# Kernel tuning notes

Measured on AMD Instinct MI355X. Metric: run time of the kernel, lower is better.

Reference implementation:

```python
import jax, jax.numpy as jnp
import numpy as np

B, CIN, COUT, H, W = 8, 64, 64, 32, 64


def _conv3x3(x, w, b):
    # x: [B,Cin,H,W], w: [Cout,Cin,3,3], b: [Cout]; SAME padding (pad=1)
    y = jax.lax.conv_general_dilated(
        x, w, window_strides=(1, 1), padding=((1, 1), (1, 1)),
        dimension_numbers=('NCHW', 'OIHW', 'NCHW'))
    return y + b[None, :, None, None]


def setup_inputs() -> dict:
    key = jax.random.key(0)
    ks = jax.random.split(key, 7)
    fan_in = CIN * 3 * 3
    s = 1.0 / np.sqrt(fan_in)
    x = jax.random.normal(ks[0], (B, CIN, H, W), dtype=jnp.float32)
    wq = jax.random.uniform(ks[1], (COUT, CIN, 3, 3), jnp.float32, -s, s)
    bq = jax.random.uniform(ks[2], (COUT,), jnp.float32, -s, s)
    wk = jax.random.uniform(ks[3], (COUT, CIN, 3, 3), jnp.float32, -s, s)
    bk = jax.random.uniform(ks[4], (COUT,), jnp.float32, -s, s)
    wv = jax.random.uniform(ks[5], (COUT, CIN, 3, 3), jnp.float32, -s, s)
    bv = jax.random.uniform(ks[6], (COUT,), jnp.float32, -s, s)
    return {"x": x, "wq": wq, "bq": bq, "wk": wk, "bk": bk, "wv": wv, "bv": bv}


def reference(x, wq, bq, wk, bk, wv, bv):
    b, _, h, w = x.shape
    n = h * w
    q = _conv3x3(x, wq, bq).reshape(b, COUT, n)  # [B,C,N]
    k = _conv3x3(x, wk, bk).reshape(b, COUT, n)
    v = _conv3x3(x, wv, bv).reshape(b, COUT, n)
    # scores[b, i, j] = sum_c q[b,c,i] * k[b,c,j]  (NOTE: no 1/sqrt(d) scaling, as in source)
    scores = jnp.einsum('bci,bcj->bij', q, k)      # [B,N,N]
    attn = jax.nn.softmax(scores, axis=-1)
    out = jnp.einsum('bij,bcj->bci', attn, v)      # attn @ V^T, then transpose -> [B,C,N]
    return out.reshape(b, COUT, h, w)
```

## Files before the change

### kernel.cpp

```cpp
#include <hip/hip_runtime.h>
#include <hip/hip_bf16.h>

#define BATCH 8
#define NC    64
#define HH    32
#define WW    64
#define NN    2048
#define NCP   72
#define NCHUNK 4
#define KVBLK 64

typedef __attribute__((ext_vector_type(8))) short bf16x8;
typedef __attribute__((ext_vector_type(4))) short short4v;
typedef __attribute__((ext_vector_type(4))) float f32x4;

__device__ __forceinline__ unsigned short f2bf(float f) {
    union { float f; unsigned u; } v; v.f = f;
    unsigned r = v.u + 0x7fffu + ((v.u >> 16) & 1u);
    return (unsigned short)(r >> 16);
}
__device__ __forceinline__ float bf2f(unsigned short h) {
    union { unsigned u; float f; } v; v.u = ((unsigned)h) << 16;
    return v.f;
}

__device__ __forceinline__ bf16x8 load8(const unsigned short* a, const unsigned short* b) {
    short4v lo = *(const short4v*)a;
    short4v hi = *(const short4v*)b;
    return __builtin_shufflevector(lo, hi, 0, 1, 2, 3, 4, 5, 6, 7);
}

__device__ __forceinline__ int ci_of_slot(int j) {
    return (j & 32) | (((j >> 2) & 1) << 4) | (((j >> 3) & 3) << 2) | (j & 3);
}

__global__ __launch_bounds__(256) void prep_w(
    const float* __restrict__ wq, const float* __restrict__ wk,
    const float* __restrict__ wv, unsigned short* __restrict__ wb)
{
    const int idx = blockIdx.x * 256 + threadIdx.x;
    if (idx >= 9 * 192 * 64) return;
    const int j    = idx & 63;
    const int row  = (idx >> 6) % 192;
    const int tap  = idx / (192 * 64);
    const int ci   = ci_of_slot(j);
    const int conv = row >> 6;
    const int cout = row & 63;
    const float* ww = (conv == 0) ? wq : (conv == 1) ? wk : wv;
    wb[idx] = f2bf(ww[((size_t)cout * 64 + ci) * 9 + tap]);
}

__global__ __launch_bounds__(256) void prep_x(
    const float* __restrict__ x, unsigned short* __restrict__ xb)
{
    __shared__ unsigned short T[64][72];
    const int bi  = blockIdx.x >> 5;
    const int y   = blockIdx.x & 31;
    const int tid = threadIdx.x;

#pragma unroll
    for (int pass = 0; pass < 16; ++pass) {
        const int idx = pass * 256 + tid;
        const int ci = idx >> 6, xx = idx & 63;
        T[xx][ci] = f2bf(x[(((size_t)bi * 64 + ci) * 32 + y) * 64 + xx]);
    }
    __syncthreads();

#pragma unroll
    for (int pass = 0; pass < 2; ++pass) {
        const int chunk = pass * 256 + tid;
        const int xx = chunk >> 3, j8 = chunk & 7;
        unsigned short h[8];
#pragma unroll
        for (int e = 0; e < 8; ++e)
            h[e] = T[xx][ci_of_slot(j8 * 8 + e)];
        uint4 u;
        u.x = (unsigned)h[0] | ((unsigned)h[1] << 16);
        u.y = (unsigned)h[2] | ((unsigned)h[3] << 16);
        u.z = (unsigned)h[4] | ((unsigned)h[5] << 16);
        u.w = (unsigned)h[6] | ((unsigned)h[7] << 16);
        *(uint4*)(xb + ((((size_t)bi * 32 + y) * 64 + xx) * 64) + j8 * 8) = u;
    }
}

__global__ __launch_bounds__(256) void conv_mfma(
    const unsigned short* __restrict__ xb,
    const unsigned short* __restrict__ wb,
    const float* __restrict__ bq, const float* __restrict__ bk,
    const float* __restrict__ bv,
    unsigned short* __restrict__ qT,
    unsigned short* __restrict__ kT,
    unsigned short* __restrict__ vv)
{
    __shared__ __align__(16) unsigned short Xs[3][66][NCP];
    __shared__ __align__(16) unsigned short Ws[2][96][NCP];

    const int bid = blockIdx.x;
    const int bi  = bid >> 6;
    const int rem = bid & 63;
    const int y   = rem >> 1;
    const int h   = rem & 1;
    const int tid = threadIdx.x;
    const int l   = tid & 63;
    const int w   = tid >> 6;
    const int g   = l >> 4;
    const int li  = l & 15;
    const int mq  = w & 1;
    const int pp  = w >> 1;

#pragma unroll
    for (int r = 0; r < 3; ++r) {
        const int yy = y + r - 1;
#pragma unroll
        for (int pass = 0; pass < 3; ++pass) {
            const int chunk = pass * 256 + tid;
            if (chunk >= 528) break;
            const int c = chunk >> 3, ci8 = chunk & 7;
            uint4 d = {0, 0, 0, 0};
            const int xx = c - 1;
            if (yy >= 0 && yy < HH && xx >= 0 && xx < WW)
                d = *(const uint4*)(xb + ((((size_t)bi * HH + yy) * WW + xx) * 64) + ci8 * 8);
            *(uint4*)&Xs[r][c][ci8 * 8] = d;
        }
    }
#pragma unroll
    for (int pass = 0; pass < 3; ++pass) {
        const int chunk = pass * 256 + tid;
        const int row = chunk >> 3, ci8 = chunk & 7;
        uint4 d = *(const uint4*)(wb + ((size_t)(h * 96 + row)) * 64 + ci8 * 8);
        *(uint4*)&Ws[0][row][ci8 * 8] = d;
    }
    __syncthreads();

    f32x4 acc[2][3];
#pragma unroll
    for (int p2 = 0; p2 < 2; ++p2)
#pragma unroll
        for (int ct = 0; ct < 3; ++ct) acc[p2][ct] = (f32x4){0, 0, 0, 0};

#pragma unroll
    for (int tap = 0; tap < 9; ++tap) {
        const int ky = tap / 3, kx = tap % 3;
        const int cur = tap & 1;

        uint4 wd[3];
        if (tap < 8) {
#pragma unroll
            for (int pass = 0; pass < 3; ++pass) {
                const int chunk = pass * 256 + tid;
                const int row = chunk >> 3, ci8 = chunk & 7;
                wd[pass] = *(const uint4*)(wb + ((size_t)(tap + 1) * 192 + h * 96 + row) * 64 + ci8 * 8);
            }
        }

        bf16x8 xf[2][2];
#pragma unroll
        for (int p2 = 0; p2 < 2; ++p2) {
            const int c = pp * 32 + p2 * 16 + li + kx;
            xf[p2][0] = *(const bf16x8*)&Xs[ky][c][g * 8];
            xf[p2][1] = *(const bf16x8*)&Xs[ky][c][32 + g * 8];
        }

#pragma unroll
        for (int ct = 0; ct < 3; ++ct) {
            const int row = mq * 48 + ct * 16 + li;
            const bf16x8 wf0 = *(const bf16x8*)&Ws[cur][row][g * 8];
            const bf16x8 wf1 = *(const bf16x8*)&Ws[cur][row][32 + g * 8];
            acc[0][ct] = __builtin_amdgcn_mfma_f32_16x16x32_bf16(wf0, xf[0][0], acc[0][ct], 0, 0, 0);
            acc[0][ct] = __builtin_amdgcn_mfma_f32_16x16x32_bf16(wf1, xf[0][1], acc[0][ct], 0, 0, 0);
            acc[1][ct] = __builtin_amdgcn_mfma_f32_16x16x32_bf16(wf0, xf[1][0], acc[1][ct], 0, 0, 0);
            acc[1][ct] = __builtin_amdgcn_mfma_f32_16x16x32_bf16(wf1, xf[1][1], acc[1][ct], 0, 0, 0);
        }

        if (tap < 8) {
#pragma unroll
            for (int pass = 0; pass < 3; ++pass) {
                const int chunk = pass * 256 + tid;
                const int row = chunk >> 3, ci8 = chunk & 7;
                *(uint4*)&Ws[cur ^ 1][row][ci8 * 8] = wd[pass];
            }
            __syncthreads();
        }
    }

#pragma unroll
    for (int p2 = 0; p2 < 2; ++p2) {
        const int n = y * 64 + pp * 32 + p2 * 16 + li;
#pragma unroll
        for (int ct = 0; ct < 3; ++ct) {
            const int rowbase = h * 96 + mq * 48 + ct * 16 + 4 * g;
            const int conv  = rowbase >> 6;
            const int cout0 = rowbase & 63;
            const float* bias = (conv == 0) ? bq : (conv == 1) ? bk : bv;
            float v0 = acc[p2][ct][0] + bias[cout0 + 0];
            float v1 = acc[p2][ct][1] + bias[cout0 + 1];
            float v2 = acc[p2][ct][2] + bias[cout0 + 2];
            float v3 = acc[p2][ct][3] + bias[cout0 + 3];
            if (conv < 2) {
                uint2 pk;
                pk.x = (unsigned)f2bf(v0) | ((unsigned)f2bf(v1) << 16);
                pk.y = (unsigned)f2bf(v2) | ((unsigned)f2bf(v3) << 16);
                unsigned short* dst = ((conv == 0) ? qT : kT) +
                                      ((size_t)bi * NN + n) * NC + cout0;
                *(uint2*)dst = pk;
            } else {
                vv[((size_t)bi * NC + cout0 + 0) * NN + n] = f2bf(v0);
                vv[((size_t)bi * NC + cout0 + 1) * NN + n] = f2bf(v1);
                vv[((size_t)bi * NC + cout0 + 2) * NN + n] = f2bf(v2);
                vv[((size_t)bi * NC + cout0 + 3) * NN + n] = f2bf(v3);
            }
        }
    }
}

__global__ __launch_bounds__(256) void attn_mfma_split(
    const unsigned short* __restrict__ qT,
    const unsigned short* __restrict__ kT,
    const unsigned short* __restrict__ vv,
    unsigned short* __restrict__ Po,
    float* __restrict__ Pm, float* __restrict__ Pl)
{
    __shared__ __align__(16) unsigned short Ks[2][KVBLK][72];
    __shared__ __align__(16) unsigned short Vs[2][64][72];

    const int bid  = blockIdx.x;
    const int g8   = bid & 7;
    const int s    = bid >> 3;
    const int qq   = s >> 5;
    const int it   = s & 31;
    const int G    = g8 + 8 * qq;
    const int bi   = G >> 2;
    const int chunk= G & 3;

    const int tid = threadIdx.x;
    const int l   = tid & 63;
    const int w   = tid >> 6;
    const int g   = l >> 4;
    const int li  = l & 15;
    const int i0  = it * 64;
    const int jbase = chunk * (NN / NCHUNK);
    const int NT  = (NN / NCHUNK) / KVBLK;

    const unsigned short* qb = qT + (size_t)bi * NN * NC;
    const unsigned short* kb = kT + (size_t)bi * NN * NC;
    const unsigned short* vb = vv + (size_t)bi * NC * NN;

    const int qrow = i0 + w * 16 + li;
    const bf16x8 qf0 = load8(qb + (size_t)qrow * NC + 4 * g,      qb + (size_t)qrow * NC + 16 + 4 * g);
    const bf16x8 qf1 = load8(qb + (size_t)qrow * NC + 32 + 4 * g, qb + (size_t)qrow * NC + 48 + 4 * g);

    uint4 kd[2], vd[2];
#pragma unroll
    for (int u = 0; u < 2; ++u) {
        const int chunkid = u * 256 + tid;
        const int r = chunkid >> 3, c8 = chunkid & 7;
        kd[u] = *(const uint4*)(kb + ((size_t)(jbase + r)) * NC + c8 * 8);
        vd[u] = *(const uint4*)(vb + (size_t)r * NN + jbase + c8 * 8);
        *(uint4*)&Ks[0][r][c8 * 8] = kd[u];
        *(uint4*)&Vs[0][r][c8 * 8] = vd[u];
    }
    __syncthreads();

    f32x4 o0 = {0,0,0,0}, o1 = {0,0,0,0}, o2 = {0,0,0,0}, o3 = {0,0,0,0};
    float m = -1e30f, lsum = 0.0f;

    for (int t = 0; t < NT; ++t) {
        const int cur = t & 1;
        if (t < NT - 1) {
            const int j0 = jbase + (t + 1) * KVBLK;
#pragma unroll
            for (int u = 0; u < 2; ++u) {
                const int chunkid = u * 256 + tid;
                const int r = chunkid >> 3, c8 = chunkid & 7;
                kd[u] = *(const uint4*)(kb + ((size_t)(j0 + r)) * NC + c8 * 8);
                vd[u] = *(const uint4*)(vb + (size_t)r * NN + j0 + c8 * 8);
            }
        }

        f32x4 d[4];
        __builtin_amdgcn_s_setprio(1);
#pragma unroll
        for (int jb = 0; jb < 4; ++jb) {
            const bf16x8 kfa = load8(&Ks[cur][jb * 16 + li][4 * g],      &Ks[cur][jb * 16 + li][16 + 4 * g]);
            const bf16x8 kfb = load8(&Ks[cur][jb * 16 + li][32 + 4 * g], &Ks[cur][jb * 16 + li][48 + 4 * g]);
            const f32x4 z = {0,0,0,0};
            d[jb] = __builtin_amdgcn_mfma_f32_16x16x32_bf16(kfa, qf0, z, 0, 0, 0);
            d[jb] = __builtin_amdgcn_mfma_f32_16x16x32_bf16(kfb, qf1, d[jb], 0, 0, 0);
        }
        __builtin_amdgcn_s_setprio(0);

        float p[16];
#pragma unroll
        for (int jb = 0; jb < 4; ++jb)
#pragma unroll
            for (int e = 0; e < 4; ++e) p[jb * 4 + e] = d[jb][e];

        float pmax = p[0];
#pragma unroll
        for (int e = 1; e < 16; ++e) pmax = fmaxf(pmax, p[e]);
        pmax = fmaxf(pmax, __shfl_xor(pmax, 16));
        pmax = fmaxf(pmax, __shfl_xor(pmax, 32));

        if (!__all(pmax <= m)) {
            const float mn = fmaxf(m, pmax);
            const float alpha = __expf(m - mn);
            m = mn;
#pragma unroll
            for (int r = 0; r < 4; ++r) {
                const float ar = __shfl(alpha, 4 * g + r, 16);
                o0[r] *= ar; o1[r] *= ar; o2[r] *= ar; o3[r] *= ar;
            }
            lsum *= alpha;
        }

        float ls = 0.0f;
#pragma unroll
        for (int e = 0; e < 16; ++e) {
            p[e] = __expf(p[e] - m);
            ls += p[e];
        }
        ls += __shfl_xor(ls, 16);
        ls += __shfl_xor(ls, 32);
        lsum += ls;

        bf16x8 pf0, pf1;
#pragma unroll
        for (int e = 0; e < 8; ++e) {
            pf0[e] = (short)f2bf(p[e]);
            pf1[e] = (short)f2bf(p[8 + e]);
        }

        __builtin_amdgcn_s_setprio(1);
        {
            const bf16x8 va0 = load8(&Vs[cur][li][4 * g],      &Vs[cur][li][16 + 4 * g]);
            const bf16x8 va1 = load8(&Vs[cur][li][32 + 4 * g], &Vs[cur][li][48 + 4 * g]);
            o0 = __builtin_amdgcn_mfma_f32_16x16x32_bf16(pf0, va0, o0, 0, 0, 0);
            o0 = __builtin_amdgcn_mfma_f32_16x16x32_bf16(pf1, va1, o0, 0, 0, 0);
            const bf16x8 vb0 = load8(&Vs[cur][16 + li][4 * g],      &Vs[cur][16 + li][16 + 4 * g]);
            const bf16x8 vb1 = load8(&Vs[cur][16 + li][32 + 4 * g], &Vs[cur][16 + li][48 + 4 * g]);
            o1 = __builtin_amdgcn_mfma_f32_16x16x32_bf16(pf0, vb0, o1, 0, 0, 0);
            o1 = __builtin_amdgcn_mfma_f32_16x16x32_bf16(pf1, vb1, o1, 0, 0, 0);
            const bf16x8 vc0 = load8(&Vs[cur][32 + li][4 * g],      &Vs[cur][32 + li][16 + 4 * g]);
            const bf16x8 vc1 = load8(&Vs[cur][32 + li][32 + 4 * g], &Vs[cur][32 + li][48 + 4 * g]);
            o2 = __builtin_amdgcn_mfma_f32_16x16x32_bf16(pf0, vc0, o2, 0, 0, 0);
            o2 = __builtin_amdgcn_mfma_f32_16x16x32_bf16(pf1, vc1, o2, 0, 0, 0);
            const bf16x8 vd0 = load8(&Vs[cur][48 + li][4 * g],      &Vs[cur][48 + li][16 + 4 * g]);
            const bf16x8 vd1 = load8(&Vs[cur][48 + li][32 + 4 * g], &Vs[cur][48 + li][48 + 4 * g]);
            o3 = __builtin_amdgcn_mfma_f32_16x16x32_bf16(pf0, vd0, o3, 0, 0, 0);
            o3 = __builtin_amdgcn_mfma_f32_16x16x32_bf16(pf1, vd1, o3, 0, 0, 0);
        }
        __builtin_amdgcn_s_setprio(0);

        if (t < NT - 1) {
#pragma unroll
            for (int u = 0; u < 2; ++u) {
                const int chunkid = u * 256 + tid;
                const int r = chunkid >> 3, c8 = chunkid & 7;
                *(uint4*)&Ks[cur ^ 1][r][c8 * 8] = kd[u];
                *(uint4*)&Vs[cur ^ 1][r][c8 * 8] = vd[u];
            }
        }
        __syncthreads();
    }

    unsigned short* pob = Po + (((size_t)chunk * BATCH + bi) * NN) * NC;
#pragma unroll
    for (int r = 0; r < 4; ++r) {
        const int row = i0 + w * 16 + 4 * g + r;
        uint2 pk;
        pk.x = (unsigned)f2bf(o0[r]) | ((unsigned)f2bf(o1[r]) << 16);
        pk.y = (unsigned)f2bf(o2[r]) | ((unsigned)f2bf(o3[r]) << 16);
        *(uint2*)(pob + (size_t)row * NC + 4 * li) = pk;
    }
    if (g == 0) {
        const size_t mi = ((size_t)chunk * BATCH + bi) * NN + i0 + w * 16 + li;
        Pm[mi] = m;
        Pl[mi] = lsum;
    }
}

__global__ __launch_bounds__(256) void attn_combine(
    const unsigned short* __restrict__ Po,
    const float* __restrict__ Pm, const float* __restrict__ Pl,
    float* __restrict__ out)
{
    __shared__ float wf[NCHUNK][64];
    __shared__ float Os[64][66];

    const int bi = blockIdx.x >> 5;
    const int it = blockIdx.x & 31;
    const int i0 = it * 64;
    const int tid = threadIdx.x;

    {
        const int ch = tid >> 6, i = tid & 63;
        wf[ch][i] = Pm[((size_t)ch * BATCH + bi) * NN + i0 + i];
    }
    __syncthreads();
    if (tid < 64) {
        float mv[NCHUNK];
        float ms = -1e30f;
#pragma unroll
        for (int ch = 0; ch < NCHUNK; ++ch) {
            mv[ch] = wf[ch][tid];
            ms = fmaxf(ms, mv[ch]);
        }
        float denom = 0.0f;
        float ev[NCHUNK];
#pragma unroll
        for (int ch = 0; ch < NCHUNK; ++ch) {
            ev[ch] = __expf(mv[ch] - ms);
            denom = fmaf(ev[ch], Pl[((size_t)ch * BATCH + bi) * NN + i0 + tid], denom);
        }
        const float inv = 1.0f / denom;
#pragma unroll
        for (int ch = 0; ch < NCHUNK; ++ch)
            wf[ch][tid] = ev[ch] * inv;
    }
    __syncthreads();

    {
        const int rg = tid >> 6, ss = tid & 63;
        const int c = (ss & 3) * 16 + (ss >> 2);
#pragma unroll
        for (int k = 0; k < 16; ++k) {
            const int i = rg * 16 + k;
            float acc = 0.0f;
#pragma unroll
            for (int ch = 0; ch < NCHUNK; ++ch) {
                const float pv = bf2f(Po[(((size_t)ch * BATCH + bi) * NN + i0 + i) * NC + ss]);
                acc = fmaf(wf[ch][i], pv, acc);
            }
            Os[i][c] = acc;
        }
    }
    __syncthreads();

    {
        const int c = tid & 63, rg = tid >> 6;
        float* ob = out + ((size_t)bi * NC + c) * NN + i0 + rg * 16;
        float tmp[16];
#pragma unroll
        for (int k = 0; k < 16; ++k) tmp[k] = Os[rg * 16 + k][c];
#pragma unroll
        for (int k = 0; k < 16; k += 4)
            *(float4*)(ob + k) = make_float4(tmp[k], tmp[k+1], tmp[k+2], tmp[k+3]);
    }
}

extern "C" void kernel_launch(void* const* d_in, const int* in_sizes, int n_in,
                              void* d_out, int out_size, void* d_ws, size_t ws_size,
                              hipStream_t stream)
{
    const float* x  = (const float*)d_in[0];
    const float* wq = (const float*)d_in[1];
    const float* bq = (const float*)d_in[2];
    const float* wk = (const float*)d_in[3];
    const float* bk = (const float*)d_in[4];
    const float* wv = (const float*)d_in[5];
    const float* bv = (const float*)d_in[6];

    unsigned short* ws16 = (unsigned short*)d_ws;
    const size_t TEN = (size_t)BATCH * NN * NC;
    unsigned short* qT = ws16;
    unsigned short* kT = ws16 + TEN;
    unsigned short* vv = ws16 + 2 * TEN;
    unsigned short* xb = ws16 + 3 * TEN;
    unsigned short* wb = ws16 + 4 * TEN;
    unsigned short* Po = ws16 + 4 * TEN + 131072;
    float* Pm = (float*)(ws16 + 4 * TEN + 131072 + (size_t)NCHUNK * TEN);
    float* Pl = Pm + (size_t)NCHUNK * BATCH * NN;
    float* out = (float*)d_out;

    prep_w<<<dim3(432), 256, 0, stream>>>(wq, wk, wv, wb);
    prep_x<<<dim3(256), 256, 0, stream>>>(x, xb);
    conv_mfma<<<dim3(512), 256, 0, stream>>>(xb, wb, bq, bk, bv, qT, kT, vv);
    attn_mfma_split<<<dim3(BATCH * 32 * NCHUNK), 256, 0, stream>>>(qT, kT, vv, Po, Pm, Pl);
    attn_combine<<<dim3(BATCH * 32), 256, 0, stream>>>(Po, Pm, Pl, out);
}
```

Baseline: 57.84 us.

## Merge prep kernels and split conv and combine into smaller blocks for occupancy

Merges the weight and input preparation kernels into one launch. The input transpose now uses half-row tiles, so that launch has 944 blocks. The convolution kernel now covers half a row per block, giving 1024 blocks. The combine kernel handles 16 query rows per block instead of 64, giving 4x more blocks. The aim is to cut one launch and to fill more compute units on small stages, at the cost of more redundant halo loads and more repeated weight tile loads per output.

```diff
diff --git a/kernel.cpp b/kernel.cpp
--- a/kernel.cpp
+++ b/kernel.cpp
@@ -34,52 +34,55 @@
     return (j & 32) | (((j >> 2) & 1) << 4) | (((j >> 3) & 3) << 2) | (j & 3);
 }
 
-__global__ __launch_bounds__(256) void prep_w(
+__global__ __launch_bounds__(256) void prep_wx(
     const float* __restrict__ wq, const float* __restrict__ wk,
-    const float* __restrict__ wv, unsigned short* __restrict__ wb)
+    const float* __restrict__ wv, const float* __restrict__ x,
+    unsigned short* __restrict__ wb, unsigned short* __restrict__ xb)
 {
-    const int idx = blockIdx.x * 256 + threadIdx.x;
-    if (idx >= 9 * 192 * 64) return;
-    const int j    = idx & 63;
-    const int row  = (idx >> 6) % 192;
-    const int tap  = idx / (192 * 64);
-    const int ci   = ci_of_slot(j);
-    const int conv = row >> 6;
-    const int cout = row & 63;
-    const float* ww = (conv == 0) ? wq : (conv == 1) ? wk : wv;
-    wb[idx] = f2bf(ww[((size_t)cout * 64 + ci) * 9 + tap]);
-}
-
-__global__ __launch_bounds__(256) void prep_x(
-    const float* __restrict__ x, unsigned short* __restrict__ xb)
-{
-    __shared__ unsigned short T[64][72];
-    const int bi  = blockIdx.x >> 5;
-    const int y   = blockIdx.x & 31;
+    __shared__ unsigned short T[32][72];
+    const int bid = blockIdx.x;
     const int tid = threadIdx.x;
 
-#pragma unroll
-    for (int pass = 0; pass < 16; ++pass) {
+    if (bid < 432) {
+        const int idx = bid * 256 + tid;
+        if (idx >= 9 * 192 * 64) return;
+        const int j    = idx & 63;
+        const int row  = (idx >> 6) % 192;
+        const int tap  = idx / (192 * 64);
+        const int ci   = ci_of_slot(j);
+        const int conv = row >> 6;
+        const int cout = row & 63;
+        const float* ww = (conv == 0) ? wq : (conv == 1) ? wk : wv;
+        wb[idx] = f2bf(ww[((size_t)cout * 64 + ci) * 9 + tap]);
+        return;
+    }
+
+    const int bid2 = bid - 432;
+    const int bi   = bid2 >> 6;
+    const int rem  = bid2 & 63;
+    const int y    = rem >> 1;
+    const int x0   = (rem & 1) * 32;
+
+#pragma unroll
+    for (int pass = 0; pass < 8; ++pass) {
         const int idx = pass * 256 + tid;
-        const int ci = idx >> 6, xx = idx & 63;
-        T[xx][ci] = f2bf(x[(((size_t)bi * 64 + ci) * 32 + y) * 64 + xx]);
-    }
-    __syncthreads();
-
-#pragma unroll
-    for (int pass = 0; pass < 2; ++pass) {
-        const int chunk = pass * 256 + tid;
-        const int xx = chunk >> 3, j8 = chunk & 7;
+        const int ci = idx >> 5, xx0 = idx & 31;
+        T[xx0][ci] = f2bf(x[(((size_t)bi * 64 + ci) * 32 + y) * 64 + x0 + xx0]);
+    }
+    __syncthreads();
+
+    {
+        const int xx0 = tid >> 3, j8 = tid & 7;
         unsigned short h[8];
 #pragma unroll
         for (int e = 0; e < 8; ++e)
-            h[e] = T[xx][ci_of_slot(j8 * 8 + e)];
+            h[e] = T[xx0][ci_of_slot(j8 * 8 + e)];
         uint4 u;
         u.x = (unsigned)h[0] | ((unsigned)h[1] << 16);
         u.y = (unsigned)h[2] | ((unsigned)h[3] << 16);
         u.z = (unsigned)h[4] | ((unsigned)h[5] << 16);
         u.w = (unsigned)h[6] | ((unsigned)h[7] << 16);
-        *(uint4*)(xb + ((((size_t)bi * 32 + y) * 64 + xx) * 64) + j8 * 8) = u;
+        *(uint4*)(xb + ((((size_t)bi * 32 + y) * 64 + x0 + xx0) * 64) + j8 * 8) = u;
     }
 }
 
@@ -92,13 +95,14 @@
     unsigned short* __restrict__ kT,
     unsigned short* __restrict__ vv)
 {
-    __shared__ __align__(16) unsigned short Xs[3][66][NCP];
+    __shared__ __align__(16) unsigned short Xs[3][34][NCP];
     __shared__ __align__(16) unsigned short Ws[2][96][NCP];
 
     const int bid = blockIdx.x;
-    const int bi  = bid >> 6;
-    const int rem = bid & 63;
-    const int y   = rem >> 1;
+    const int bi  = bid >> 7;
+    const int rem = bid & 127;
+    const int y   = rem >> 2;
+    const int xh  = (rem >> 1) & 1;
     const int h   = rem & 1;
     const int tid = threadIdx.x;
     const int l   = tid & 63;
@@ -107,17 +111,18 @@
     const int li  = l & 15;
     const int mq  = w & 1;
     const int pp  = w >> 1;
-
-#pragma unroll
-    for (int r = 0; r < 3; ++r) {
-        const int yy = y + r - 1;
-#pragma unroll
-        for (int pass = 0; pass < 3; ++pass) {
-            const int chunk = pass * 256 + tid;
-            if (chunk >= 528) break;
-            const int c = chunk >> 3, ci8 = chunk & 7;
+    const int x0  = xh * 32;
+
+#pragma unroll
+    for (int pass = 0; pass < 4; ++pass) {
+        const int chunk = pass * 256 + tid;
+        if (chunk < 816) {
+            const int r  = chunk / 272;
+            const int cc = chunk % 272;
+            const int c  = cc >> 3, ci8 = cc & 7;
+            const int yy = y + r - 1;
+            const int xx = x0 + c - 1;
             uint4 d = {0, 0, 0, 0};
-            const int xx = c - 1;
             if (yy >= 0 && yy < HH && xx >= 0 && xx < WW)
                 d = *(const uint4*)(xb + ((((size_t)bi * HH + yy) * WW + xx) * 64) + ci8 * 8);
             *(uint4*)&Xs[r][c][ci8 * 8] = d;
@@ -132,11 +137,9 @@
     }
     __syncthreads();
 
-    f32x4 acc[2][3];
-#pragma unroll
-    for (int p2 = 0; p2 < 2; ++p2)
-#pragma unroll
-        for (int ct = 0; ct < 3; ++ct) acc[p2][ct] = (f32x4){0, 0, 0, 0};
+    f32x4 acc[3];
+#pragma unroll
+    for (int ct = 0; ct < 3; ++ct) acc[ct] = (f32x4){0, 0, 0, 0};
 
 #pragma unroll
     for (int tap = 0; tap < 9; ++tap) {
@@ -153,23 +156,17 @@
             }
         }
 
-        bf16x8 xf[2][2];
-#pragma unroll
-        for (int p2 = 0; p2 < 2; ++p2) {
-            const int c = pp * 32 + p2 * 16 + li + kx;
-            xf[p2][0] = *(const bf16x8*)&Xs[ky][c][g * 8];
-            xf[p2][1] = *(const bf16x8*)&Xs[ky][c][32 + g * 8];
-        }
+        const int c = pp * 16 + li + kx;
+        const bf16x8 xf0 = *(const bf16x8*)&Xs[ky][c][g * 8];
+        const bf16x8 xf1 = *(const bf16x8*)&Xs[ky][c][32 + g * 8];
 
 #pragma unroll
         for (int ct = 0; ct < 3; ++ct) {
             const int row = mq * 48 + ct * 16 + li;
             const bf16x8 wf0 = *(const bf16x8*)&Ws[cur][row][g * 8];
             const bf16x8 wf1 = *(const bf16x8*)&Ws[cur][row][32 + g * 8];
-            acc[0][ct] = __builtin_amdgcn_mfma_f32_16x16x32_bf16(wf0, xf[0][0], acc[0][ct], 0, 0, 0);
-            acc[0][ct] = __builtin_amdgcn_mfma_f32_16x16x32_bf16(wf1, xf[0][1], acc[0][ct], 0, 0, 0);
-            acc[1][ct] = __builtin_amdgcn_mfma_f32_16x16x32_bf16(wf0, xf[1][0], acc[1][ct], 0, 0, 0);
-            acc[1][ct] = __builtin_amdgcn_mfma_f32_16x16x32_bf16(wf1, xf[1][1], acc[1][ct], 0, 0, 0);
+            acc[ct] = __builtin_amdgcn_mfma_f32_16x16x32_bf16(wf0, xf0, acc[ct], 0, 0, 0);
+            acc[ct] = __builtin_amdgcn_mfma_f32_16x16x32_bf16(wf1, xf1, acc[ct], 0, 0, 0);
         }
 
         if (tap < 8) {
@@ -183,32 +180,29 @@
         }
     }
 
-#pragma unroll
-    for (int p2 = 0; p2 < 2; ++p2) {
-        const int n = y * 64 + pp * 32 + p2 * 16 + li;
-#pragma unroll
-        for (int ct = 0; ct < 3; ++ct) {
-            const int rowbase = h * 96 + mq * 48 + ct * 16 + 4 * g;
-            const int conv  = rowbase >> 6;
-            const int cout0 = rowbase & 63;
-            const float* bias = (conv == 0) ? bq : (conv == 1) ? bk : bv;
-            float v0 = acc[p2][ct][0] + bias[cout0 + 0];
-            float v1 = acc[p2][ct][1] + bias[cout0 + 1];
-            float v2 = acc[p2][ct][2] + bias[cout0 + 2];
-            float v3 = acc[p2][ct][3] + bias[cout0 + 3];
-            if (conv < 2) {
-                uint2 pk;
-                pk.x = (unsigned)f2bf(v0) | ((unsigned)f2bf(v1) << 16);
-                pk.y = (unsigned)f2bf(v2) | ((unsigned)f2bf(v3) << 16);
-                unsigned short* dst = ((conv == 0) ? qT : kT) +
-                                      ((size_t)bi * NN + n) * NC + cout0;
-                *(uint2*)dst = pk;
-            } else {
-                vv[((size_t)bi * NC + cout0 + 0) * NN + n] = f2bf(v0);
-                vv[((size_t)bi * NC + cout0 + 1) * NN + n] = f2bf(v1);
-                vv[((size_t)bi * NC + cout0 + 2) * NN + n] = f2bf(v2);
-                vv[((size_t)bi * NC + cout0 + 3) * NN + n] = f2bf(v3);
-            }
+    const int n = y * 64 + x0 + pp * 16 + li;
+#pragma unroll
+    for (int ct = 0; ct < 3; ++ct) {
+        const int rowbase = h * 96 + mq * 48 + ct * 16 + 4 * g;
+        const int conv  = rowbase >> 6;
+        const int cout0 = rowbase & 63;
+        const float* bias = (conv == 0) ? bq : (conv == 1) ? bk : bv;
+        float v0 = acc[ct][0] + bias[cout0 + 0];
+        float v1 = acc[ct][1] + bias[cout0 + 1];
+        float v2 = acc[ct][2] + bias[cout0 + 2];
+        float v3 = acc[ct][3] + bias[cout0 + 3];
+        if (conv < 2) {
+            uint2 pk;
+            pk.x = (unsigned)f2bf(v0) | ((unsigned)f2bf(v1) << 16);
+            pk.y = (unsigned)f2bf(v2) | ((unsigned)f2bf(v3) << 16);
+            unsigned short* dst = ((conv == 0) ? qT : kT) +
+                                  ((size_t)bi * NN + n) * NC + cout0;
+            *(uint2*)dst = pk;
+        } else {
+            vv[((size_t)bi * NC + cout0 + 0) * NN + n] = f2bf(v0);
+            vv[((size_t)bi * NC + cout0 + 1) * NN + n] = f2bf(v1);
+            vv[((size_t)bi * NC + cout0 + 2) * NN + n] = f2bf(v2);
+            vv[((size_t)bi * NC + cout0 + 3) * NN + n] = f2bf(v3);
         }
     }
 }
@@ -384,20 +378,20 @@
     const float* __restrict__ Pm, const float* __restrict__ Pl,
     float* __restrict__ out)
 {
-    __shared__ float wf[NCHUNK][64];
-    __shared__ float Os[64][66];
-
-    const int bi = blockIdx.x >> 5;
-    const int it = blockIdx.x & 31;
-    const int i0 = it * 64;
+    __shared__ float wf[NCHUNK][16];
+    __shared__ float Os[16][66];
+
+    const int bi = blockIdx.x >> 7;
+    const int it = blockIdx.x & 127;
+    const int i0 = it * 16;
     const int tid = threadIdx.x;
 
-    {
-        const int ch = tid >> 6, i = tid & 63;
-        wf[ch][i] = Pm[((size_t)ch * BATCH + bi) * NN + i0 + i];
-    }
-    __syncthreads();
     if (tid < 64) {
+        const int ch = tid >> 4, il = tid & 15;
+        wf[ch][il] = Pm[((size_t)ch * BATCH + bi) * NN + i0 + il];
+    }
+    __syncthreads();
+    if (tid < 16) {
         float mv[NCHUNK];
         float ms = -1e30f;
 #pragma unroll
@@ -423,8 +417,8 @@
         const int rg = tid >> 6, ss = tid & 63;
         const int c = (ss & 3) * 16 + (ss >> 2);
 #pragma unroll
-        for (int k = 0; k < 16; ++k) {
-            const int i = rg * 16 + k;
+        for (int k = 0; k < 4; ++k) {
+            const int i = rg * 4 + k;
             float acc = 0.0f;
 #pragma unroll
             for (int ch = 0; ch < NCHUNK; ++ch) {
@@ -438,13 +432,9 @@
 
     {
         const int c = tid & 63, rg = tid >> 6;
-        float* ob = out + ((size_t)bi * NC + c) * NN + i0 + rg * 16;
-        float tmp[16];
-#pragma unroll
-        for (int k = 0; k < 16; ++k) tmp[k] = Os[rg * 16 + k][c];
-#pragma unroll
-        for (int k = 0; k < 16; k += 4)
-            *(float4*)(ob + k) = make_float4(tmp[k], tmp[k+1], tmp[k+2], tmp[k+3]);
+        float* ob = out + ((size_t)bi * NC + c) * NN + i0 + rg * 4;
+        *(float4*)ob = make_float4(Os[rg * 4 + 0][c], Os[rg * 4 + 1][c],
+                                   Os[rg * 4 + 2][c], Os[rg * 4 + 3][c]);
     }
 }
 
@@ -472,9 +462,8 @@
     float* Pl = Pm + (size_t)NCHUNK * BATCH * NN;
     float* out = (float*)d_out;
 
-    prep_w<<<dim3(432), 256, 0, stream>>>(wq, wk, wv, wb);
-    prep_x<<<dim3(256), 256, 0, stream>>>(x, xb);
-    conv_mfma<<<dim3(512), 256, 0, stream>>>(xb, wb, bq, bk, bv, qT, kT, vv);
+    prep_wx<<<dim3(944), 256, 0, stream>>>(wq, wk, wv, x, wb, xb);
+    conv_mfma<<<dim3(1024), 256, 0, stream>>>(xb, wb, bq, bk, bv, qT, kT, vv);
     attn_mfma_split<<<dim3(BATCH * 32 * NCHUNK), 256, 0, stream>>>(qT, kT, vv, Po, Pm, Pl);
-    attn_combine<<<dim3(BATCH * 32), 256, 0, stream>>>(Po, Pm, Pl, out);
-}
+    attn_combine<<<dim3(BATCH * 128), 256, 0, stream>>>(Po, Pm, Pl, out);
+}
```

Result: no change. 56.79 us (-1.8%).
